# Kernel tuning notes

Hardware: AMD Instinct MI355X
Metric: run time of the kernel (lower is better)

The kernel has to match this reference:

```python
import jax, jax.numpy as jnp
import numpy as np

IN, H, C, B = 1024, 1024, 16, 4096


def setup_inputs() -> dict:
    key = jax.random.key(0)
    ks = jax.random.split(key, 5)
    s = 1.0 / np.sqrt(IN)
    sh = 1.0 / np.sqrt(H)
    return {
        "input_word": jax.random.normal(ks[0], (B, IN), dtype=jnp.float32),
        "hidden_states": jax.random.normal(ks[1], (B, H), dtype=jnp.float32),
        # stacked per-cell Linear weights (torch Linear: y = x @ W.T + b)
        "Wx": jax.random.uniform(ks[2], (C, 2 * H, IN), jnp.float32, -s, s),
        "bx": jax.random.uniform(ks[3], (C, 2 * H), jnp.float32, -s, s),
        "Wh": jax.random.uniform(ks[4], (C, 2 * H, H), jnp.float32, -sh, sh),
    }


def reference(input_word, hidden_states, Wx, bx, Wh):
    # all cells active (entity_mask all ones, domain_tag='Source')
    # net[b,c,o] = sum_i x[b,i] Wx[c,o,i] + bx[c,o] + sum_h h[b,h] Wh[c,o,h]
    net = (jnp.einsum('bi,coi->bco', input_word, Wx)
           + jnp.einsum('bh,coh->bco', hidden_states, Wh)
           + bx[None, :, :])  # [B, C, 2H]
    input_gate, cell_states = net[..., :H], net[..., H:]
    cell_input = jnp.tanh(cell_states)
    input_gate = jax.nn.sigmoid(input_gate)
    return (cell_input, input_gate)
```

## Files before the change

### kernel.cpp

```cpp
#include <hip/hip_runtime.h>
#include <hip/hip_bf16.h>

#define IN_DIM 1024
#define H_DIM  1024
#define C_DIM  16
#define B_DIM  4096
#define K_DIM  2048
#define N_DIM  32768
#define M_DIM  4096
#define NKT    64

typedef __attribute__((ext_vector_type(8))) short short8;
typedef __attribute__((ext_vector_type(4))) float f32x4;

__device__ __forceinline__ unsigned short f2bf_rne(float f) {
  union { float f; unsigned u; } a; a.f = f;
  unsigned r = a.u + 0x7FFFu + ((a.u >> 16) & 1u);
  return (unsigned short)(r >> 16);
}

__global__ void convert_pack_kernel(const float* __restrict__ xs,
                                    const float* __restrict__ hs,
                                    unsigned short* __restrict__ out,
                                    int rows) {
  long total = (long)rows * (K_DIM / 8);
  for (long i = blockIdx.x * (long)blockDim.x + threadIdx.x; i < total;
       i += (long)gridDim.x * blockDim.x) {
    long e = i * 8;
    int r = (int)(e >> 11);
    int k = (int)(e & 2047);
    const float* src = (k < IN_DIM) ? (xs + (long)r * IN_DIM + k)
                                    : (hs + (long)r * H_DIM + (k - IN_DIM));
    float4 v0 = *(const float4*)(src);
    float4 v1 = *(const float4*)(src + 4);
    union { unsigned short u[8]; short8 s; } p;
    p.u[0] = f2bf_rne(v0.x); p.u[1] = f2bf_rne(v0.y);
    p.u[2] = f2bf_rne(v0.z); p.u[3] = f2bf_rne(v0.w);
    p.u[4] = f2bf_rne(v1.x); p.u[5] = f2bf_rne(v1.y);
    p.u[6] = f2bf_rne(v1.z); p.u[7] = f2bf_rne(v1.w);
    *(short8*)(out + e) = p.s;
  }
}

__device__ __forceinline__ void gload_lds16(const void* g, void* l) {
  __builtin_amdgcn_global_load_lds(
      (const __attribute__((address_space(1))) unsigned int*)g,
      (__attribute__((address_space(3))) unsigned int*)l, 16, 0, 0);
}

__global__ void __launch_bounds__(512, 2)
gemm_act_kernel(const short* __restrict__ A,
                const short* __restrict__ Bt,
                const float* __restrict__ bias,
                float* __restrict__ out) {
  extern __shared__ short lds[];
  short* sA0 = lds;          short* sB0 = lds + 24576;
  short* sA1 = lds + 8192;   short* sB1 = lds + 32768;
  short* sA2 = lds + 16384;  short* sB2 = lds + 40960;

  int cpx = (int)gridDim.x >> 3;
  int wg  = ((int)blockIdx.x & 7) * cpx + ((int)blockIdx.x >> 3);
  int mt = wg & 15;
  int nt = wg >> 4;
  int m0 = mt * 256;
  int n0 = nt * 256;

  const int tid  = (int)threadIdx.x;
  const int lane = tid & 63;
  const int wid  = tid >> 6;
  const int wr   = wid >> 2;
  const int wc   = wid & 3;

  const int srow = tid >> 2;
  const int schk = (tid & 3) ^ ((tid >> 3) & 3);
  const long gA0 = (long)(m0 + srow) * K_DIM + schk * 8;
  const long gB0 = (long)(n0 + srow) * K_DIM + schk * 8;
  const int  lo0 = tid * 8;
  const int  lo1 = tid * 8 + 4096;

  auto stageA = [&](int kt, short* dst) {
    const short* g = A + gA0 + (long)kt * 32;
    gload_lds16(g,                      dst + lo0);
    gload_lds16(g + (long)128 * K_DIM,  dst + lo1);
  };
  auto stageB = [&](int kt, short* dst) {
    const short* g = Bt + gB0 + (long)kt * 32;
    gload_lds16(g,                      dst + lo0);
    gload_lds16(g + (long)128 * K_DIM,  dst + lo1);
  };

  const int fr = lane & 15;
  const int g8 = lane >> 4;
  int aoff[8], boff[4];
#pragma unroll
  for (int mi = 0; mi < 8; ++mi) {
    int row = wr * 128 + mi * 16 + fr;
    aoff[mi] = row * 32 + ((g8 ^ ((row >> 1) & 3)) << 3);
  }
#pragma unroll
  for (int ni = 0; ni < 4; ++ni) {
    int row = wc * 64 + ni * 16 + fr;
    boff[ni] = row * 32 + ((g8 ^ ((row >> 1) & 3)) << 3);
  }

  f32x4 acc[8][4] = {};

  stageA(0, sA0); stageB(0, sB0);
  stageA(1, sA1); stageB(1, sB1);
  asm volatile("s_waitcnt vmcnt(4)" ::: "memory");
  __builtin_amdgcn_s_barrier();

  short* cA = sA0; short* cB = sB0;
  short* nA = sA1; short* nB = sB1;
  short* pA = sA2; short* pB = sB2;

  for (int t = 0; t < NKT; ++t) {
    short8 av[4], bv[4];
    if (t < NKT - 2) stageA(t + 2, pA);
#pragma unroll
    for (int i = 0; i < 4; ++i) av[i] = *(const short8*)(cA + aoff[i]);
#pragma unroll
    for (int i = 0; i < 4; ++i) bv[i] = *(const short8*)(cB + boff[i]);
    __builtin_amdgcn_s_barrier();
    __builtin_amdgcn_s_setprio(1);
#pragma unroll
    for (int i = 0; i < 4; ++i)
#pragma unroll
      for (int j = 0; j < 4; ++j)
        acc[i][j] = __builtin_amdgcn_mfma_f32_16x16x32_bf16(av[i], bv[j], acc[i][j], 0, 0, 0);
    __builtin_amdgcn_s_setprio(0);
    __builtin_amdgcn_s_barrier();
    if (t < NKT - 2) stageB(t + 2, pB);
#pragma unroll
    for (int i = 0; i < 4; ++i) av[i] = *(const short8*)(cA + aoff[4 + i]);
    __builtin_amdgcn_s_barrier();
    __builtin_amdgcn_s_setprio(1);
#pragma unroll
    for (int i = 0; i < 4; ++i)
#pragma unroll
      for (int j = 0; j < 4; ++j)
        acc[4 + i][j] = __builtin_amdgcn_mfma_f32_16x16x32_bf16(av[i], bv[j], acc[4 + i][j], 0, 0, 0);
    __builtin_amdgcn_s_setprio(0);
    if (t < NKT - 2) asm volatile("s_waitcnt vmcnt(4)" ::: "memory");
    else             asm volatile("s_waitcnt vmcnt(0)" ::: "memory");
    __builtin_amdgcn_s_barrier();
    short* tAp = cA; cA = nA; nA = pA; pA = tAp;
    short* tBp = cB; cB = nB; nB = pB; pB = tBp;
  }

  const int crow = (lane >> 4) * 4;
  const int ccol = lane & 15;
  const long HALF = (long)B_DIM * C_DIM * H_DIM;
  float bia[4]; int cg[4], og[4];
#pragma unroll
  for (int ni = 0; ni < 4; ++ni) {
    int gn = n0 + wc * 64 + ni * 16 + ccol;
    bia[ni] = bias[gn];
    cg[ni] = gn >> 11;
    og[ni] = gn & 2047;
  }
#pragma unroll
  for (int mi = 0; mi < 8; ++mi) {
    int gb0 = m0 + wr * 128 + mi * 16 + crow;
#pragma unroll
    for (int ni = 0; ni < 4; ++ni) {
      int c = cg[ni], o = og[ni];
#pragma unroll
      for (int j = 0; j < 4; ++j) {
        float v = acc[mi][ni][j] + bia[ni];
        long b = gb0 + j;
        if (o < H_DIM) {
          float r = 1.0f / (1.0f + __expf(-v));
          __builtin_nontemporal_store(r, &out[HALF + (b * C_DIM + c) * H_DIM + o]);
        } else {
          float av2 = fabsf(v);
          float e = __expf(-2.0f * av2);
          float r = (1.0f - e) / (1.0f + e);
          r = (v < 0.0f) ? -r : r;
          __builtin_nontemporal_store(r, &out[(b * C_DIM + c) * H_DIM + (o - H_DIM)]);
        }
      }
    }
  }
}

__global__ void fallback_kernel(const float* __restrict__ x,
                                const float* __restrict__ h,
                                const float* __restrict__ Wx,
                                const float* __restrict__ bx,
                                const float* __restrict__ Wh,
                                float* __restrict__ out) {
  int b = blockIdx.x;
  int c = blockIdx.y;
  __shared__ float lx[IN_DIM], lh[H_DIM];
  for (int i = threadIdx.x; i < IN_DIM; i += blockDim.x) {
    lx[i] = x[(long)b * IN_DIM + i];
    lh[i] = h[(long)b * H_DIM + i];
  }
  __syncthreads();
  const long HALF = (long)B_DIM * C_DIM * H_DIM;
  for (int o = threadIdx.x; o < 2 * H_DIM; o += blockDim.x) {
    const float* wx = Wx + ((long)c * 2 * H_DIM + o) * IN_DIM;
    const float* wh = Wh + ((long)c * 2 * H_DIM + o) * H_DIM;
    float acc = bx[c * 2 * H_DIM + o];
    for (int k = 0; k < IN_DIM; ++k) acc += lx[k] * wx[k];
    for (int k = 0; k < H_DIM; ++k) acc += lh[k] * wh[k];
    if (o < H_DIM) {
      out[HALF + ((long)b * C_DIM + c) * H_DIM + o] = 1.0f / (1.0f + __expf(-acc));
    } else {
      float av = fabsf(acc);
      float t = __expf(-2.0f * av);
      float r = (1.0f - t) / (1.0f + t);
      out[((long)b * C_DIM + c) * H_DIM + (o - H_DIM)] = (acc < 0.0f) ? -r : r;
    }
  }
}

extern "C" void kernel_launch(void* const* d_in, const int* in_sizes, int n_in,
                              void* d_out, int out_size, void* d_ws, size_t ws_size,
                              hipStream_t stream) {
  const float* x  = (const float*)d_in[0];
  const float* h  = (const float*)d_in[1];
  const float* Wx = (const float*)d_in[2];
  const float* bx = (const float*)d_in[3];
  const float* Wh = (const float*)d_in[4];
  float* out = (float*)d_out;

  const size_t needA = (size_t)M_DIM * K_DIM * sizeof(short);
  const size_t needB = (size_t)N_DIM * K_DIM * sizeof(short);
  if (ws_size < needA + needB) {
    dim3 g(B_DIM, C_DIM);
    fallback_kernel<<<g, 256, 0, stream>>>(x, h, Wx, bx, Wh, out);
    return;
  }

  unsigned short* Abf = (unsigned short*)d_ws;
  unsigned short* Bbf = (unsigned short*)((char*)d_ws + needA);

  convert_pack_kernel<<<2048, 256, 0, stream>>>(x, h, Abf, M_DIM);
  convert_pack_kernel<<<4096, 256, 0, stream>>>(Wx, Wh, Bbf, N_DIM);

  (void)hipFuncSetAttribute((const void*)gemm_act_kernel,
                            hipFuncAttributeMaxDynamicSharedMemorySize, 98304);
  gemm_act_kernel<<<2048, 512, 98304, stream>>>((const short*)Abf, (const short*)Bbf,
                                                bx, out);
}
```

Baseline: 826.7 us.

## Use 64-wide K tiles with double-buffered LDS and interleaved partial staging

Doubles the K-tile depth from 32 to 64, halving the number of main-loop iterations and barrier rounds. Three 32-wide buffers become two 64-wide buffers, with next-tile loads split into row quarters issued between the MFMA phases. The XOR swizzle changes to an 8-chunk pattern to match the wider rows. LDS use rises from 96KB to 128KB per block, which can cut occupancy (launch bounds ask for 2 blocks of 512 threads). Buffer reuse ordering becomes more delicate.

```diff
diff --git a/kernel.cpp b/kernel.cpp
--- a/kernel.cpp
+++ b/kernel.cpp
@@ -8,7 +8,7 @@
 #define K_DIM  2048
 #define N_DIM  32768
 #define M_DIM  4096
-#define NKT    64
+#define NT     32
 
 typedef __attribute__((ext_vector_type(8))) short short8;
 typedef __attribute__((ext_vector_type(4))) float f32x4;
@@ -54,9 +54,10 @@
                 const float* __restrict__ bias,
                 float* __restrict__ out) {
   extern __shared__ short lds[];
-  short* sA0 = lds;          short* sB0 = lds + 24576;
-  short* sA1 = lds + 8192;   short* sB1 = lds + 32768;
-  short* sA2 = lds + 16384;  short* sB2 = lds + 40960;
+  short* sA0 = lds;
+  short* sA1 = lds + 16384;
+  short* sB0 = lds + 32768;
+  short* sB1 = lds + 49152;
 
   int cpx = (int)gridDim.x >> 3;
   int wg  = ((int)blockIdx.x & 7) * cpx + ((int)blockIdx.x >> 3);
@@ -71,81 +72,109 @@
   const int wr   = wid >> 2;
   const int wc   = wid & 3;
 
-  const int srow = tid >> 2;
-  const int schk = (tid & 3) ^ ((tid >> 3) & 3);
-  const long gA0 = (long)(m0 + srow) * K_DIM + schk * 8;
-  const long gB0 = (long)(n0 + srow) * K_DIM + schk * 8;
-  const int  lo0 = tid * 8;
-  const int  lo1 = tid * 8 + 4096;
-
-  auto stageA = [&](int kt, short* dst) {
-    const short* g = A + gA0 + (long)kt * 32;
-    gload_lds16(g,                      dst + lo0);
-    gload_lds16(g + (long)128 * K_DIM,  dst + lo1);
+  const int srow = tid >> 3;
+  const int sc   = (tid & 7) ^ (srow & 7);
+  const long gAoff = (long)(m0 + srow) * K_DIM + sc * 8;
+  const long gBoff = (long)(n0 + srow) * K_DIM + sc * 8;
+  const int  dOff  = srow * 64 + (tid & 7) * 8;
+
+  auto stageA = [&](int kt, int r0, short* dst) {
+    gload_lds16(A + gAoff + (long)r0 * K_DIM + kt * 64, dst + r0 * 64 + dOff);
   };
-  auto stageB = [&](int kt, short* dst) {
-    const short* g = Bt + gB0 + (long)kt * 32;
-    gload_lds16(g,                      dst + lo0);
-    gload_lds16(g + (long)128 * K_DIM,  dst + lo1);
+  auto stageB = [&](int kt, int r0, short* dst) {
+    gload_lds16(Bt + gBoff + (long)r0 * K_DIM + kt * 64, dst + r0 * 64 + dOff);
   };
 
   const int fr = lane & 15;
   const int g8 = lane >> 4;
-  int aoff[8], boff[4];
+  int aoff[8][2], boff[4][2];
 #pragma unroll
   for (int mi = 0; mi < 8; ++mi) {
-    int row = wr * 128 + mi * 16 + fr;
-    aoff[mi] = row * 32 + ((g8 ^ ((row >> 1) & 3)) << 3);
+    int r = wr * 128 + mi * 16 + fr;
+#pragma unroll
+    for (int kk = 0; kk < 2; ++kk)
+      aoff[mi][kk] = r * 64 + (((kk * 4 + g8) ^ (r & 7)) << 3);
   }
 #pragma unroll
   for (int ni = 0; ni < 4; ++ni) {
-    int row = wc * 64 + ni * 16 + fr;
-    boff[ni] = row * 32 + ((g8 ^ ((row >> 1) & 3)) << 3);
+    int r = wc * 64 + ni * 16 + fr;
+#pragma unroll
+    for (int kk = 0; kk < 2; ++kk)
+      boff[ni][kk] = r * 64 + (((kk * 4 + g8) ^ (r & 7)) << 3);
   }
 
   f32x4 acc[8][4] = {};
 
-  stageA(0, sA0); stageB(0, sB0);
-  stageA(1, sA1); stageB(1, sB1);
-  asm volatile("s_waitcnt vmcnt(4)" ::: "memory");
+  stageB(0, 0, sB0); stageB(0, 64, sB0); stageB(0, 128, sB0); stageB(0, 192, sB0);
+  stageA(0, 0, sA0); stageA(0, 128, sA0); stageA(0, 64, sA0); stageA(0, 192, sA0);
+  stageB(1, 0, sB1); stageB(1, 64, sB1); stageB(1, 128, sB1); stageB(1, 192, sB1);
+  stageA(1, 0, sA1); stageA(1, 128, sA1);
+  asm volatile("s_waitcnt vmcnt(6)" ::: "memory");
   __builtin_amdgcn_s_barrier();
 
-  short* cA = sA0; short* cB = sB0;
-  short* nA = sA1; short* nB = sB1;
-  short* pA = sA2; short* pB = sB2;
-
-  for (int t = 0; t < NKT; ++t) {
-    short8 av[4], bv[4];
-    if (t < NKT - 2) stageA(t + 2, pA);
-#pragma unroll
-    for (int i = 0; i < 4; ++i) av[i] = *(const short8*)(cA + aoff[i]);
-#pragma unroll
-    for (int i = 0; i < 4; ++i) bv[i] = *(const short8*)(cB + boff[i]);
-    __builtin_amdgcn_s_barrier();
-    __builtin_amdgcn_s_setprio(1);
-#pragma unroll
-    for (int i = 0; i < 4; ++i)
-#pragma unroll
-      for (int j = 0; j < 4; ++j)
-        acc[i][j] = __builtin_amdgcn_mfma_f32_16x16x32_bf16(av[i], bv[j], acc[i][j], 0, 0, 0);
-    __builtin_amdgcn_s_setprio(0);
-    __builtin_amdgcn_s_barrier();
-    if (t < NKT - 2) stageB(t + 2, pB);
-#pragma unroll
-    for (int i = 0; i < 4; ++i) av[i] = *(const short8*)(cA + aoff[4 + i]);
-    __builtin_amdgcn_s_barrier();
-    __builtin_amdgcn_s_setprio(1);
-#pragma unroll
-    for (int i = 0; i < 4; ++i)
-#pragma unroll
-      for (int j = 0; j < 4; ++j)
-        acc[4 + i][j] = __builtin_amdgcn_mfma_f32_16x16x32_bf16(av[i], bv[j], acc[4 + i][j], 0, 0, 0);
-    __builtin_amdgcn_s_setprio(0);
-    if (t < NKT - 2) asm volatile("s_waitcnt vmcnt(4)" ::: "memory");
-    else             asm volatile("s_waitcnt vmcnt(0)" ::: "memory");
-    __builtin_amdgcn_s_barrier();
-    short* tAp = cA; cA = nA; nA = pA; pA = tAp;
-    short* tBp = cB; cB = nB; nB = pB; pB = tBp;
+  auto iter = [&](int t, short* cA, short* cB, short* nA) {
+    const bool s1 = (t + 1) < NT;
+    const bool s2 = (t + 2) < NT;
+    short8 av0[4], av1[4], bv0[4], bv1[4];
+    if (s1) { stageA(t + 1, 64, nA); stageA(t + 1, 192, nA); }
+#pragma unroll
+    for (int i = 0; i < 4; ++i) av0[i] = *(const short8*)(cA + aoff[i][0]);
+#pragma unroll
+    for (int j = 0; j < 4; ++j) bv0[j] = *(const short8*)(cB + boff[j][0]);
+#pragma unroll
+    for (int j = 0; j < 4; ++j) bv1[j] = *(const short8*)(cB + boff[j][1]);
+    __builtin_amdgcn_s_barrier();
+    __builtin_amdgcn_s_setprio(1);
+#pragma unroll
+    for (int i = 0; i < 4; ++i)
+#pragma unroll
+      for (int j = 0; j < 4; ++j)
+        acc[i][j] = __builtin_amdgcn_mfma_f32_16x16x32_bf16(av0[i], bv0[j], acc[i][j], 0, 0, 0);
+    __builtin_amdgcn_s_setprio(0);
+    __builtin_amdgcn_s_barrier();
+    if (s2) { stageB(t + 2, 0, cB); stageB(t + 2, 64, cB); }
+#pragma unroll
+    for (int i = 0; i < 4; ++i) av1[i] = *(const short8*)(cA + aoff[i][1]);
+    __builtin_amdgcn_s_barrier();
+    __builtin_amdgcn_s_setprio(1);
+#pragma unroll
+    for (int i = 0; i < 4; ++i)
+#pragma unroll
+      for (int j = 0; j < 4; ++j)
+        acc[i][j] = __builtin_amdgcn_mfma_f32_16x16x32_bf16(av1[i], bv1[j], acc[i][j], 0, 0, 0);
+    __builtin_amdgcn_s_setprio(0);
+    __builtin_amdgcn_s_barrier();
+    if (s2) { stageB(t + 2, 128, cB); stageB(t + 2, 192, cB); }
+#pragma unroll
+    for (int i = 0; i < 4; ++i) av0[i] = *(const short8*)(cA + aoff[4 + i][0]);
+    __builtin_amdgcn_s_barrier();
+    __builtin_amdgcn_s_setprio(1);
+#pragma unroll
+    for (int i = 0; i < 4; ++i)
+#pragma unroll
+      for (int j = 0; j < 4; ++j)
+        acc[4 + i][j] = __builtin_amdgcn_mfma_f32_16x16x32_bf16(av0[i], bv0[j], acc[4 + i][j], 0, 0, 0);
+    __builtin_amdgcn_s_setprio(0);
+    __builtin_amdgcn_s_barrier();
+    if (s2) { stageA(t + 2, 0, cA); stageA(t + 2, 128, cA); }
+#pragma unroll
+    for (int i = 0; i < 4; ++i) av1[i] = *(const short8*)(cA + aoff[4 + i][1]);
+    __builtin_amdgcn_s_barrier();
+    __builtin_amdgcn_s_setprio(1);
+#pragma unroll
+    for (int i = 0; i < 4; ++i)
+#pragma unroll
+      for (int j = 0; j < 4; ++j)
+        acc[4 + i][j] = __builtin_amdgcn_mfma_f32_16x16x32_bf16(av1[i], bv1[j], acc[4 + i][j], 0, 0, 0);
+    __builtin_amdgcn_s_setprio(0);
+    if (s2) asm volatile("s_waitcnt vmcnt(6)" ::: "memory");
+    else    asm volatile("s_waitcnt vmcnt(0)" ::: "memory");
+    __builtin_amdgcn_s_barrier();
+  };
+
+  for (int t = 0; t < NT; t += 2) {
+    iter(t,     sA0, sB0, sA1);
+    iter(t + 1, sA1, sB1, sA0);
   }
 
   const int crow = (lane >> 4) * 4;
@@ -241,7 +270,7 @@
   convert_pack_kernel<<<4096, 256, 0, stream>>>(Wx, Wh, Bbf, N_DIM);
 
   (void)hipFuncSetAttribute((const void*)gemm_act_kernel,
-                            hipFuncAttributeMaxDynamicSharedMemorySize, 98304);
-  gemm_act_kernel<<<2048, 512, 98304, stream>>>((const short*)Abf, (const short*)Bbf,
-                                                bx, out);
-}
+                            hipFuncAttributeMaxDynamicSharedMemorySize, 131072);
+  gemm_act_kernel<<<2048, 512, 131072, stream>>>((const short*)Abf, (const short*)Bbf,
+                                                 bx, out);
+}
```

New measurement: 775.1 us. -6.2%, faster.
